# Optimization experiments

Measured on AMD Instinct MI355X. Metric: run time of the kernel, lower is better.

## Reference

```python
import math
import jax, jax.numpy as jnp
import numpy as np

B, S, D_MODEL, H = 8, 1024, 512, 8
HEAD = D_MODEL // H
MAX_REL = 16


def rel_index(length_q, length_k):
    # clipped relative-position index matrix [Lq, Lk] in [0, 2*MAX_REL]
    rq = jnp.arange(length_q)
    rk = jnp.arange(length_k)
    dist = rk[None, :] - rq[:, None]
    return jnp.clip(dist, -MAX_REL, MAX_REL) + MAX_REL


def setup_inputs() -> dict:
    key = jax.random.key(0)
    ks = jax.random.split(key, 13)
    sc = 1.0 / math.sqrt(D_MODEL)
    inp = {
        "query": jax.random.normal(ks[0], (B, S, D_MODEL), jnp.float32),
        "key": jax.random.normal(ks[1], (B, S, D_MODEL), jnp.float32),
        "value": jax.random.normal(ks[2], (B, S, D_MODEL), jnp.float32),
        "Wq": jax.random.normal(ks[3], (D_MODEL, D_MODEL), jnp.float32) * sc,
        "bq": jnp.zeros((D_MODEL,), jnp.float32),
        "Wk": jax.random.normal(ks[4], (D_MODEL, D_MODEL), jnp.float32) * sc,
        "bk": jnp.zeros((D_MODEL,), jnp.float32),
        "Wv": jax.random.normal(ks[5], (D_MODEL, D_MODEL), jnp.float32) * sc,
        "bv": jnp.zeros((D_MODEL,), jnp.float32),
        "Wo": jax.random.normal(ks[6], (D_MODEL, D_MODEL), jnp.float32) * sc,
        "bo": jnp.zeros((D_MODEL,), jnp.float32),
        "rel_k_table": jax.random.normal(ks[7], (2 * MAX_REL + 1, HEAD), jnp.float32),
        "rel_v_table": jax.random.normal(ks[8], (2 * MAX_REL + 1, HEAD), jnp.float32),
    }
    return inp


def reference(query, key, value, Wq, bq, Wk, bk, Wv, bv, Wo, bo, rel_k_table, rel_v_table):
    b, s, d = query.shape
    # input projections (torch Linear: x @ W.T + b)
    q = query @ Wq.T + bq  # [B,S,D]
    k = key @ Wk.T + bk
    v = value @ Wv.T + bv
    # split heads: [B,H,S,HEAD]
    qh = q.reshape(b, s, H, HEAD).transpose(0, 2, 1, 3)
    kh = k.reshape(b, s, H, HEAD).transpose(0, 2, 1, 3)
    vh = v.reshape(b, s, H, HEAD).transpose(0, 2, 1, 3)
    # content-content scores
    attn1 = jnp.einsum("bhqd,bhkd->bhqk", qh, kh)
    # content-position scores via gathered relative embeddings [S,S,HEAD]
    idx = rel_index(s, s)
    rk = rel_k_table[idx]
    attn2 = jnp.einsum("bhqd,qkd->bhqk", qh, rk)
    # NOTE: original code scales by sqrt(batch_size), reproduced faithfully
    scale = math.sqrt(float(B))
    attn = jax.nn.softmax((attn1 + attn2) / scale, axis=-1)
    # values: content + relative-position value term
    w1 = jnp.einsum("bhqk,bhkd->bhqd", attn, vh)
    rv = rel_v_table[idx]
    w2 = jnp.einsum("bhqk,qkd->bhqd", attn, rv)
    x = (w1 + w2).transpose(0, 2, 1, 3).reshape(b * s, d)
    return x @ Wo.T + bo
```

## Files before the change

kernel.cpp:

```cpp
#include <hip/hip_runtime.h>

typedef unsigned short u16;
typedef float f32x4 __attribute__((ext_vector_type(4)));
typedef float f32x16 __attribute__((ext_vector_type(16)));
typedef __bf16 bf16x8 __attribute__((ext_vector_type(8)));

#define MFMA16(a, b, c) __builtin_amdgcn_mfma_f32_16x16x32_bf16((a), (b), (c), 0, 0, 0)
#define MFMA32(a, b, c) __builtin_amdgcn_mfma_f32_32x32x16_bf16((a), (b), (c), 0, 0, 0)

#define B_ 8
#define H_ 8
#define S_ 1024

__device__ __forceinline__ u16 f2bf(float f) {
  unsigned u = __float_as_uint(f);
  return (u16)((u + 0x7fffu + ((u >> 16) & 1u)) >> 16);
}
__device__ __forceinline__ unsigned cvtpk(float a, float b) {
  unsigned r;
  asm("v_cvt_pk_bf16_f32 %0, %1, %2" : "=v"(r) : "v"(a), "v"(b));
  return r;
}
__device__ __forceinline__ void plswap(unsigned& a, unsigned& b) {
  asm("v_permlane32_swap_b32 %0, %1" : "+v"(a), "+v"(b));
}
__device__ __forceinline__ void gload16(const void* g, void* l) {
  __builtin_amdgcn_global_load_lds((__attribute__((address_space(1))) const void*)g,
                                   (__attribute__((address_space(3))) void*)l, 16, 0, 0);
}

__global__ void __launch_bounds__(256) convAll(const float* __restrict__ q, const float* __restrict__ k,
                                               const float* __restrict__ v, const float* __restrict__ Wq,
                                               const float* __restrict__ Wk, const float* __restrict__ Wv,
                                               const float* __restrict__ Wo, const float* __restrict__ relk,
                                               u16* __restrict__ dq, u16* __restrict__ dk, u16* __restrict__ dv,
                                               u16* __restrict__ dWq, u16* __restrict__ dWk, u16* __restrict__ dWv,
                                               u16* __restrict__ dWo, u16* __restrict__ drelk) {
  const int bid = blockIdx.x;
  const float* s; u16* d; size_t off;
  if (bid < 12288) {
    size_t i4 = (size_t)bid * 256 + threadIdx.x;
    int tsel = (int)(i4 >> 20);
    off = (i4 & 1048575) << 2;
    s = tsel == 0 ? q : (tsel == 1 ? k : v);
    d = tsel == 0 ? dq : (tsel == 1 ? dk : dv);
  } else {
    size_t i = ((size_t)(bid - 12288) * 256 + threadIdx.x) << 2;
    if (i >= 1050688) return;
    if (i < 262144)       { s = Wq; d = dWq; off = i; }
    else if (i < 524288)  { s = Wk; d = dWk; off = i - 262144; }
    else if (i < 786432)  { s = Wv; d = dWv; off = i - 524288; }
    else if (i < 1048576) { s = Wo; d = dWo; off = i - 786432; }
    else                  { s = relk; d = drelk; off = i - 1048576; }
  }
  float4 f = *(const float4*)(s + off);
  uint2 o;
  o.x = cvtpk(f.x, f.y);
  o.y = cvtpk(f.z, f.w);
  *(uint2*)(d + off) = o;
}

__global__ void __launch_bounds__(256) qkv_gemm(const u16* __restrict__ Xq, const u16* __restrict__ Xk,
                                                const u16* __restrict__ Xv, const u16* __restrict__ Wqb,
                                                const u16* __restrict__ Wkb, const u16* __restrict__ Wvb,
                                                const float* __restrict__ bq, const float* __restrict__ bk,
                                                const float* __restrict__ bv, u16* __restrict__ Qh,
                                                u16* __restrict__ Kh, u16* __restrict__ Vt) {
  __shared__ u16 As[128 * 64];
  __shared__ u16 Bs[128 * 64];
  const int seg = blockIdx.x >> 8, bid = blockIdx.x & 255;
  const u16* A = seg == 0 ? Xq : (seg == 1 ? Xk : Xv);
  const u16* W = seg == 0 ? Wqb : (seg == 1 ? Wkb : Wvb);
  const float* bias = seg == 0 ? bq : (seg == 1 ? bk : bv);
  const int tid = threadIdx.x, lane = tid & 63, wid = tid >> 6;
  const int c = lane & 15, g = lane >> 4;
  const int bm = bid >> 2, bn = bid & 3;
  const int m0 = bm << 7, n0 = bn << 7;
  const int wrow = (wid >> 1) << 6, wcol = (wid & 1) << 6;

  const f32x4 ZF = {0.f, 0.f, 0.f, 0.f};
  f32x4 acc[4][4];
#pragma unroll
  for (int i = 0; i < 4; ++i)
#pragma unroll
    for (int j = 0; j < 4; ++j) acc[i][j] = ZF;

  for (int kt = 0; kt < 512; kt += 64) {
    __syncthreads();
#pragma unroll
    for (int i = 0; i < 4; ++i) {
      int Lb = ((wid << 2) | i) << 10;
      int L = Lb + lane * 16;
      int row = L >> 7;
      int off = (L & 127) ^ ((row & 7) << 4);
      gload16((const char*)A + ((((size_t)(m0 + row)) << 9) + kt) * 2 + off, (char*)As + Lb);
      gload16((const char*)W + ((((size_t)(n0 + row)) << 9) + kt) * 2 + off, (char*)Bs + Lb);
    }
    __syncthreads();
#pragma unroll
    for (int kk = 0; kk < 2; ++kk) {
      bf16x8 af[4], bfr[4];
#pragma unroll
      for (int rt = 0; rt < 4; ++rt) {
        int row = wrow + (rt << 4) + c;
        af[rt] = *(const bf16x8*)((const char*)As + row * 128 + (((kk << 6) | (g << 4)) ^ ((row & 7) << 4)));
      }
#pragma unroll
      for (int ct = 0; ct < 4; ++ct) {
        int row = wcol + (ct << 4) + c;
        bfr[ct] = *(const bf16x8*)((const char*)Bs + row * 128 + (((kk << 6) | (g << 4)) ^ ((row & 7) << 4)));
      }
#pragma unroll
      for (int rt = 0; rt < 4; ++rt)
#pragma unroll
        for (int ct = 0; ct < 4; ++ct) acc[rt][ct] = MFMA16(af[rt], bfr[ct], acc[rt][ct]);
    }
  }

#pragma unroll
  for (int rt = 0; rt < 4; ++rt)
#pragma unroll
    for (int ct = 0; ct < 4; ++ct) {
      int n = n0 + wcol + (ct << 4) + c;
      float bv2 = bias[n];
      if (seg == 2) {
        int b2 = m0 >> 10;
        int sbase = (m0 & 1023) + wrow + (rt << 4) + (g << 2);
        int h2 = n >> 6, d2 = n & 63;
        uint2 o;
        o.x = cvtpk(acc[rt][ct][0] + bv2, acc[rt][ct][1] + bv2);
        o.y = cvtpk(acc[rt][ct][2] + bv2, acc[rt][ct][3] + bv2);
        *(uint2*)(Vt + ((((size_t)((b2 << 3) + h2) << 6) + d2) << 10) + sbase) = o;
      } else {
        u16* out = seg == 0 ? Qh : Kh;
#pragma unroll
        for (int r = 0; r < 4; ++r) {
          int m = m0 + wrow + (rt << 4) + (g << 2) + r;
          int b = m >> 10, s = m & 1023, h = n >> 6, d = n & 63;
          out[(((((size_t)(b * H_ + h)) << 10) + s) << 6) + d] = f2bf(acc[rt][ct][r] + bv2);
        }
      }
    }
}

__global__ void __launch_bounds__(256) gemm_out(const u16* __restrict__ A, const u16* __restrict__ W,
                                                const float* __restrict__ bias, float* __restrict__ out) {
  __shared__ u16 As[128 * 64];
  __shared__ u16 Bs[128 * 64];
  const int tid = threadIdx.x, lane = tid & 63, wid = tid >> 6;
  const int c = lane & 15, g = lane >> 4;
  const int bm = blockIdx.x >> 2, bn = blockIdx.x & 3;
  const int m0 = bm << 7, n0 = bn << 7;
  const int wrow = (wid >> 1) << 6, wcol = (wid & 1) << 6;

  const f32x4 ZF = {0.f, 0.f, 0.f, 0.f};
  f32x4 acc[4][4];
#pragma unroll
  for (int i = 0; i < 4; ++i)
#pragma unroll
    for (int j = 0; j < 4; ++j) acc[i][j] = ZF;

  for (int kt = 0; kt < 512; kt += 64) {
    __syncthreads();
#pragma unroll
    for (int i = 0; i < 4; ++i) {
      int Lb = ((wid << 2) | i) << 10;
      int L = Lb + lane * 16;
      int row = L >> 7;
      int off = (L & 127) ^ ((row & 7) << 4);
      gload16((const char*)A + ((((size_t)(m0 + row)) << 9) + kt) * 2 + off, (char*)As + Lb);
      gload16((const char*)W + ((((size_t)(n0 + row)) << 9) + kt) * 2 + off, (char*)Bs + Lb);
    }
    __syncthreads();
#pragma unroll
    for (int kk = 0; kk < 2; ++kk) {
      bf16x8 af[4], bfr[4];
#pragma unroll
      for (int rt = 0; rt < 4; ++rt) {
        int row = wrow + (rt << 4) + c;
        af[rt] = *(const bf16x8*)((const char*)As + row * 128 + (((kk << 6) | (g << 4)) ^ ((row & 7) << 4)));
      }
#pragma unroll
      for (int ct = 0; ct < 4; ++ct) {
        int row = wcol + (ct << 4) + c;
        bfr[ct] = *(const bf16x8*)((const char*)Bs + row * 128 + (((kk << 6) | (g << 4)) ^ ((row & 7) << 4)));
      }
#pragma unroll
      for (int rt = 0; rt < 4; ++rt)
#pragma unroll
        for (int ct = 0; ct < 4; ++ct) acc[rt][ct] = MFMA16(af[rt], bfr[ct], acc[rt][ct]);
    }
  }

#pragma unroll
  for (int rt = 0; rt < 4; ++rt)
#pragma unroll
    for (int ct = 0; ct < 4; ++ct) {
      int n = n0 + wcol + (ct << 4) + c;
      float bv = bias[n];
#pragma unroll
      for (int r = 0; r < 4; ++r) {
        int m = m0 + wrow + (rt << 4) + (g << 2) + r;
        out[(((size_t)m) << 9) + n] = acc[rt][ct][r] + bv;
      }
    }
}

__global__ void __launch_bounds__(256) flash_kernel(const u16* __restrict__ Qh, const u16* __restrict__ Kh,
                                                    const u16* __restrict__ Vt, const u16* __restrict__ relkb,
                                                    const float* __restrict__ relv, u16* __restrict__ Xout) {
  __shared__ u16 Ks[3][64 * 64];
  __shared__ u16 Vs[3][64 * 64];
  __shared__ float qrelT[33 * 128];
  __shared__ u16 Pband[128 * 32];
  __shared__ float rv32S[64];
  __shared__ float2 normS[128];

  const int tid = threadIdx.x, lane = tid & 63, wid = tid >> 6;
  const int c32 = lane & 31, hi = lane >> 5;
  const int swz = ((blockIdx.x & 7) << 6) | (blockIdx.x >> 3);
  const int bh = swz >> 3, qt = swz & 7;
  const int qbase = qt << 7;
  const size_t rowbase = ((size_t)bh) << 10;
  const int wavebase = wid << 5;
  const int qloc = wavebase + c32;
  const float K1 = 0.51013619f;
  const float C0 = 24.0f;

#define STAGE(buf_, kt_) do { \
    const int k64_ = (kt_) << 6; \
    _Pragma("unroll") \
    for (int i_ = 0; i_ < 2; ++i_) { \
      const int f_ = (wid << 1) | i_; \
      gload16((const char*)Kh + ((rowbase + k64_ + ((f_ & 1) << 5) + c32) << 7) + ((f_ >> 1) << 5) + (hi << 4), \
              (char*)Ks[buf_] + (f_ << 10)); \
      gload16((const char*)Vt + ((((size_t)(bh << 6)) + ((f_ & 1) << 5) + c32) << 11) + \
                  ((k64_ + ((f_ >> 1) << 4) + (hi << 3)) << 1), \
              (char*)Vs[buf_] + (f_ << 10)); \
    } \
  } while (0)

  STAGE(0, 0);
  STAGE(1, 1);
  STAGE(2, 2);

  ((uint4*)Pband)[tid] = uint4{0, 0, 0, 0};
  ((uint4*)Pband)[tid + 256] = uint4{0, 0, 0, 0};
  if (tid < 64) rv32S[tid] = relv[2048 + tid];

  {
    const int c = lane & 15, g = lane >> 4;
    const f32x4 ZF4 = {0.f, 0.f, 0.f, 0.f};
#pragma unroll
    for (int hf = 0; hf < 2; ++hf) {
      const int q16 = wavebase + (hf << 4) + c;
      const u16* qp = Qh + ((rowbase + qbase + q16) << 6);
      bf16x8 qa0 = *(const bf16x8*)(qp + (g << 3));
      bf16x8 qa1 = *(const bf16x8*)(qp + 32 + (g << 3));
#pragma unroll
      for (int t = 0; t < 3; ++t) {
        int rr = t * 16 + c; if (rr > 32) rr = 32;
        f32x4 qr = ZF4;
        qr = MFMA16(*(const bf16x8*)(relkb + (rr << 6) + (g << 3)), qa0, qr);
        qr = MFMA16(*(const bf16x8*)(relkb + (rr << 6) + 32 + (g << 3)), qa1, qr);
#pragma unroll
        for (int j = 0; j < 4; ++j) {
          int r = t * 16 + (g << 2) + j;
          if (r < 33) qrelT[(r << 7) + q16] = qr[j] * K1 - C0;
        }
      }
    }
  }

  bf16x8 qb[4];
  {
    const u16* qp = Qh + ((rowbase + qbase + qloc) << 6);
#pragma unroll
    for (int ks = 0; ks < 4; ++ks) qb[ks] = *(const bf16x8*)(qp + (ks << 4) + (hi << 3));
  }

  __syncthreads();

  const float bias_lo = qrelT[qloc];
  const float bias_hi = qrelT[(32 << 7) + qloc];
  const int lb16 = lane << 4;

  const f32x16 Z16 = {0.f,0.f,0.f,0.f,0.f,0.f,0.f,0.f,0.f,0.f,0.f,0.f,0.f,0.f,0.f,0.f};
  f32x16 acc0 = Z16, acc1 = Z16;
  float lsum = 0.f, lowsum = 0.f, psum = 0.f;

  int cur = 0;
  for (int kt = 0; kt < 16; ++kt) {
    f32x16 sA = Z16, sB = Z16;
    __builtin_amdgcn_s_setprio(1);
#pragma unroll
    for (int ks = 0; ks < 4; ++ks) {
      bf16x8 ka0 = *(const bf16x8*)((const char*)Ks[cur] + (((ks << 1) | 0) << 10) + lb16);
      bf16x8 ka1 = *(const bf16x8*)((const char*)Ks[cur] + (((ks << 1) | 1) << 10) + lb16);
      sA = MFMA32(ka0, qb[ks], sA);
      sB = MFMA32(ka1, qb[ks], sB);
    }
    __builtin_amdgcn_s_setprio(0);

    const int E = (kt << 6) - qbase - wavebase;
    if (E >= 48) {
      float ps[4] = {0.f, 0.f, 0.f, 0.f};
#pragma unroll
      for (int r = 0; r < 16; ++r) {
        float pe = __builtin_amdgcn_exp2f(fmaf(sA[r], K1, bias_hi)); sA[r] = pe;
        float pf = __builtin_amdgcn_exp2f(fmaf(sB[r], K1, bias_hi)); sB[r] = pf;
        ps[r & 3] += pe + pf;
      }
      lsum += (ps[0] + ps[1]) + (ps[2] + ps[3]);
    } else if (E <= -80) {
      float ps[4] = {0.f, 0.f, 0.f, 0.f};
#pragma unroll
      for (int r = 0; r < 16; ++r) {
        float pe = __builtin_amdgcn_exp2f(fmaf(sA[r], K1, bias_lo)); sA[r] = pe;
        float pf = __builtin_amdgcn_exp2f(fmaf(sB[r], K1, bias_lo)); sB[r] = pf;
        ps[r & 3] += pe + pf;
      }
      float t0 = (ps[0] + ps[1]) + (ps[2] + ps[3]);
      lsum += t0; lowsum += t0;
    } else {
      const int base = E - c32 + (hi << 2);
#pragma unroll
      for (int mt = 0; mt < 2; ++mt) {
        f32x16& s = mt ? sB : sA;
#pragma unroll
        for (int r = 0; r < 16; ++r) {
          int dlt = base + (mt << 5) + (r & 3) + ((r >> 2) << 3);
          int idx = dlt < -16 ? 0 : (dlt > 16 ? 32 : dlt + 16);
          float pe = __builtin_amdgcn_exp2f(fmaf(s[r], K1, qrelT[(idx << 7) + qloc]));
          s[r] = pe;
          lsum += pe;
          if (dlt <= -16) lowsum += pe;
          else if (dlt < 16) { psum += pe; Pband[(qloc << 5) + dlt + 16] = f2bf(pe); }
        }
      }
    }

    unsigned uA[8], uB[8];
#pragma unroll
    for (int j = 0; j < 8; ++j) {
      uA[j] = cvtpk(sA[2 * j], sA[2 * j + 1]);
      uB[j] = cvtpk(sB[2 * j], sB[2 * j + 1]);
    }
    bf16x8 pa[4];
#pragma unroll
    for (int ks = 0; ks < 4; ++ks) {
      int jb = (ks & 1) << 2;
      unsigned w0, w1, w2, w3;
      if (ks < 2) { w0 = uA[jb]; w2 = uA[jb + 2]; w1 = uA[jb + 1]; w3 = uA[jb + 3]; }
      else        { w0 = uB[jb]; w2 = uB[jb + 2]; w1 = uB[jb + 1]; w3 = uB[jb + 3]; }
      plswap(w0, w2);
      plswap(w1, w3);
      uint4 t4{w0, w1, w2, w3};
      pa[ks] = __builtin_bit_cast(bf16x8, t4);
    }

    __builtin_amdgcn_s_setprio(1);
#pragma unroll
    for (int ks = 0; ks < 4; ++ks) {
      bf16x8 vb0 = *(const bf16x8*)((const char*)Vs[cur] + (((ks << 1) | 0) << 10) + lb16);
      bf16x8 vb1 = *(const bf16x8*)((const char*)Vs[cur] + (((ks << 1) | 1) << 10) + lb16);
      acc0 = MFMA32(pa[ks], vb0, acc0);
      acc1 = MFMA32(pa[ks], vb1, acc1);
    }
    __builtin_amdgcn_s_setprio(0);

    if (kt < 15) {
      __builtin_amdgcn_s_barrier();
      __builtin_amdgcn_sched_barrier(0);
      if (kt < 13) STAGE(cur, kt + 3);
      if (kt < 13)       asm volatile("s_waitcnt vmcnt(8)" ::: "memory");
      else if (kt == 13) asm volatile("s_waitcnt vmcnt(4)" ::: "memory");
      else               asm volatile("s_waitcnt vmcnt(0)" ::: "memory");
      __builtin_amdgcn_sched_barrier(0);
      __builtin_amdgcn_s_barrier();
      __builtin_amdgcn_sched_barrier(0);
    }
    cur = (cur == 2) ? 0 : cur + 1;
  }

  lsum += __shfl_xor(lsum, 32);
  lowsum += __shfl_xor(lowsum, 32);
  psum += __shfl_xor(psum, 32);
  const float inv = 1.f / lsum;
  const float hsum = lsum - lowsum - psum;
  if (lane < 32) {
    Pband[qloc << 5] = f2bf(lowsum);
    normS[qloc] = float2{inv, hsum};
  }
  __syncthreads();
  u16* rvT = (u16*)qrelT;
  for (int i = tid; i < 2048; i += 256) rvT[i] = f2bf(relv[((i & 31) << 6) + (i >> 5)]);
  __syncthreads();

#pragma unroll
  for (int ks2 = 0; ks2 < 2; ++ks2) {
    bf16x8 pf = *(const bf16x8*)(Pband + (qloc << 5) + (ks2 << 4) + (hi << 3));
    bf16x8 rv0 = *(const bf16x8*)(rvT + (c32 << 5) + (ks2 << 4) + (hi << 3));
    bf16x8 rv1 = *(const bf16x8*)(rvT + ((32 + c32) << 5) + (ks2 << 4) + (hi << 3));
    acc0 = MFMA32(pf, rv0, acc0);
    acc1 = MFMA32(pf, rv1, acc1);
  }

  const int b = bh >> 3, h = bh & 7;
  const float rvA = rv32S[c32], rvB = rv32S[32 + c32];
#pragma unroll
  for (int r = 0; r < 16; ++r) {
    int qw = wavebase + (r & 3) + ((r >> 2) << 3) + (hi << 2);
    float2 nh = normS[qw];
    size_t orow = ((((size_t)b << 10) + (qbase + qw)) << 9) + (h << 6);
    Xout[orow + c32]      = f2bf((acc0[r] + nh.y * rvA) * nh.x);
    Xout[orow + 32 + c32] = f2bf((acc1[r] + nh.y * rvB) * nh.x);
  }
#undef STAGE
}

extern "C" void kernel_launch(void* const* d_in, const int* in_sizes, int n_in,
                              void* d_out, int out_size, void* d_ws, size_t ws_size,
                              hipStream_t stream) {
  (void)in_sizes; (void)n_in; (void)out_size; (void)ws_size;
  const float* query = (const float*)d_in[0];
  const float* key   = (const float*)d_in[1];
  const float* value = (const float*)d_in[2];
  const float* Wq = (const float*)d_in[3];
  const float* bq = (const float*)d_in[4];
  const float* Wk = (const float*)d_in[5];
  const float* bk = (const float*)d_in[6];
  const float* Wv = (const float*)d_in[7];
  const float* bv = (const float*)d_in[8];
  const float* Wo = (const float*)d_in[9];
  const float* bo = (const float*)d_in[10];
  const float* relk = (const float*)d_in[11];
  const float* relv = (const float*)d_in[12];

  char* ws = (char*)d_ws;
  u16*   Xq    = (u16*)(ws + 0);
  u16*   Xk    = (u16*)(ws + 8388608);
  u16*   Xv    = (u16*)(ws + 16777216);
  u16*   Wqb   = (u16*)(ws + 25165824);
  u16*   Wkb   = (u16*)(ws + 25690112);
  u16*   Wvb   = (u16*)(ws + 26214400);
  u16*   Wob   = (u16*)(ws + 26738688);
  u16*   relkb = (u16*)(ws + 27262976);
  u16*   Qh    = (u16*)(ws + 27271168);
  u16*   Kh    = (u16*)(ws + 35659776);
  u16*   Vt    = (u16*)(ws + 52436992);
  u16*   Xout  = (u16*)(ws + 70262784);

  convAll<<<13315, 256, 0, stream>>>(query, key, value, Wq, Wk, Wv, Wo, relk,
                                     Xq, Xk, Xv, Wqb, Wkb, Wvb, Wob, relkb);
  qkv_gemm<<<768, 256, 0, stream>>>(Xq, Xk, Xv, Wqb, Wkb, Wvb, bq, bk, bv, Qh, Kh, Vt);
  flash_kernel<<<512, 256, 0, stream>>>(Qh, Kh, Vt, relkb, relv, Xout);
  gemm_out<<<256, 256, 0, stream>>>(Xout, Wob, bo, (float*)d_out);
}
```

Before: 106.6 us.

## Load K/V tiles directly from global into registers, drop LDS triple buffer

Removes the three-stage LDS ring buffer for K and V tiles, along with its async global-to-LDS staging, vmcnt waits and per-iteration barriers. Each wave now loads its K and V MFMA operands straight from global memory (through L2/L1) into registers at the top of every key tile. This removes barrier synchronisation and frees LDS, which may raise occupancy. In exchange, the four waves no longer share K/V data through LDS, global traffic per block goes up, and load latency is no longer prefetched several tiles ahead.

```diff
diff --git a/kernel.cpp b/kernel.cpp
--- a/kernel.cpp
+++ b/kernel.cpp
@@ -209,8 +209,6 @@
 __global__ void __launch_bounds__(256) flash_kernel(const u16* __restrict__ Qh, const u16* __restrict__ Kh,
                                                     const u16* __restrict__ Vt, const u16* __restrict__ relkb,
                                                     const float* __restrict__ relv, u16* __restrict__ Xout) {
-  __shared__ u16 Ks[3][64 * 64];
-  __shared__ u16 Vs[3][64 * 64];
   __shared__ float qrelT[33 * 128];
   __shared__ u16 Pband[128 * 32];
   __shared__ float rv32S[64];
@@ -227,23 +225,6 @@
   const float K1 = 0.51013619f;
   const float C0 = 24.0f;
 
-#define STAGE(buf_, kt_) do { \
-    const int k64_ = (kt_) << 6; \
-    _Pragma("unroll") \
-    for (int i_ = 0; i_ < 2; ++i_) { \
-      const int f_ = (wid << 1) | i_; \
-      gload16((const char*)Kh + ((rowbase + k64_ + ((f_ & 1) << 5) + c32) << 7) + ((f_ >> 1) << 5) + (hi << 4), \
-              (char*)Ks[buf_] + (f_ << 10)); \
-      gload16((const char*)Vt + ((((size_t)(bh << 6)) + ((f_ & 1) << 5) + c32) << 11) + \
-                  ((k64_ + ((f_ >> 1) << 4) + (hi << 3)) << 1), \
-              (char*)Vs[buf_] + (f_ << 10)); \
-    } \
-  } while (0)
-
-  STAGE(0, 0);
-  STAGE(1, 1);
-  STAGE(2, 2);
-
   ((uint4*)Pband)[tid] = uint4{0, 0, 0, 0};
   ((uint4*)Pband)[tid + 256] = uint4{0, 0, 0, 0};
   if (tid < 64) rv32S[tid] = relv[2048 + tid];
@@ -283,26 +264,39 @@
 
   const float bias_lo = qrelT[qloc];
   const float bias_hi = qrelT[(32 << 7) + qloc];
-  const int lb16 = lane << 4;
+
+  const u16* Kbh = Kh + (rowbase << 6);
+  const u16* Vbh = Vt + ((size_t)bh << 16);
+  const u16* kp0 = Kbh + (c32 << 6) + (hi << 3);
+  const u16* vp0 = Vbh + ((size_t)c32 << 10) + (hi << 3);
 
   const f32x16 Z16 = {0.f,0.f,0.f,0.f,0.f,0.f,0.f,0.f,0.f,0.f,0.f,0.f,0.f,0.f,0.f,0.f};
   f32x16 acc0 = Z16, acc1 = Z16;
   float lsum = 0.f, lowsum = 0.f, psum = 0.f;
 
-  int cur = 0;
   for (int kt = 0; kt < 16; ++kt) {
+    const int k64 = kt << 6;
+    const u16* kp = kp0 + (k64 << 6);
+    const u16* vp = vp0 + k64;
+    bf16x8 ka0[4], ka1[4], vb0[4], vb1[4];
+#pragma unroll
+    for (int ks = 0; ks < 4; ++ks) {
+      ka0[ks] = *(const bf16x8*)(kp + (ks << 4));
+      ka1[ks] = *(const bf16x8*)(kp + 2048 + (ks << 4));
+      vb0[ks] = *(const bf16x8*)(vp + (ks << 4));
+      vb1[ks] = *(const bf16x8*)(vp + 32768 + (ks << 4));
+    }
+
     f32x16 sA = Z16, sB = Z16;
     __builtin_amdgcn_s_setprio(1);
 #pragma unroll
     for (int ks = 0; ks < 4; ++ks) {
-      bf16x8 ka0 = *(const bf16x8*)((const char*)Ks[cur] + (((ks << 1) | 0) << 10) + lb16);
-      bf16x8 ka1 = *(const bf16x8*)((const char*)Ks[cur] + (((ks << 1) | 1) << 10) + lb16);
-      sA = MFMA32(ka0, qb[ks], sA);
-      sB = MFMA32(ka1, qb[ks], sB);
+      sA = MFMA32(ka0[ks], qb[ks], sA);
+      sB = MFMA32(ka1[ks], qb[ks], sB);
     }
     __builtin_amdgcn_s_setprio(0);
 
-    const int E = (kt << 6) - qbase - wavebase;
+    const int E = k64 - qbase - wavebase;
     if (E >= 48) {
       float ps[4] = {0.f, 0.f, 0.f, 0.f};
 #pragma unroll
@@ -362,25 +356,10 @@
     __builtin_amdgcn_s_setprio(1);
 #pragma unroll
     for (int ks = 0; ks < 4; ++ks) {
-      bf16x8 vb0 = *(const bf16x8*)((const char*)Vs[cur] + (((ks << 1) | 0) << 10) + lb16);
-      bf16x8 vb1 = *(const bf16x8*)((const char*)Vs[cur] + (((ks << 1) | 1) << 10) + lb16);
-      acc0 = MFMA32(pa[ks], vb0, acc0);
-      acc1 = MFMA32(pa[ks], vb1, acc1);
+      acc0 = MFMA32(pa[ks], vb0[ks], acc0);
+      acc1 = MFMA32(pa[ks], vb1[ks], acc1);
     }
     __builtin_amdgcn_s_setprio(0);
-
-    if (kt < 15) {
-      __builtin_amdgcn_s_barrier();
-      __builtin_amdgcn_sched_barrier(0);
-      if (kt < 13) STAGE(cur, kt + 3);
-      if (kt < 13)       asm volatile("s_waitcnt vmcnt(8)" ::: "memory");
-      else if (kt == 13) asm volatile("s_waitcnt vmcnt(4)" ::: "memory");
-      else               asm volatile("s_waitcnt vmcnt(0)" ::: "memory");
-      __builtin_amdgcn_sched_barrier(0);
-      __builtin_amdgcn_s_barrier();
-      __builtin_amdgcn_sched_barrier(0);
-    }
-    cur = (cur == 2) ? 0 : cur + 1;
   }
 
   lsum += __shfl_xor(lsum, 32);
@@ -416,7 +395,6 @@
     Xout[orow + c32]      = f2bf((acc0[r] + nh.y * rvA) * nh.x);
     Xout[orow + 32 + c32] = f2bf((acc1[r] + nh.y * rvB) * nh.x);
   }
-#undef STAGE
 }
 
 extern "C" void kernel_launch(void* const* d_in, const int* in_sizes, int n_in,
```

Measured after the change: 127.8 us. +19.9%, slower.
